# Kernel optimization log

Hardware: AMD Instinct MI355X
Metric: run time of the kernel (lower is better)

## Reference

```python
import jax, jax.numpy as jnp
import numpy as np

NEG_INF = -1.0e9
LEAKY_SLOPE = 0.2


def setup_inputs() -> dict:
    key = jax.random.key(0)
    k1, k2, k3, k4, k5 = jax.random.split(key, 5)
    B, N, F_in, H, D = 4, 2048, 128, 4, 32
    x = jax.random.normal(k1, (B, N, F_in), dtype=jnp.float32)
    # binary adjacency; force self-loops so every row has >=1 neighbour
    adj = jax.random.randint(k2, (N, N), 0, 2).astype(jnp.float32)
    adj = jnp.maximum(adj, jnp.eye(N, dtype=jnp.float32))
    W = jax.random.normal(k3, (H, F_in, D), dtype=jnp.float32) * (1.0 / np.sqrt(F_in))
    a_left = jax.random.normal(k4, (H, D, 1), dtype=jnp.float32) * (1.0 / np.sqrt(D))
    a_right = jax.random.normal(k5, (H, D, 1), dtype=jnp.float32) * (1.0 / np.sqrt(D))
    bias = jnp.zeros((H, D), dtype=jnp.float32)
    return {"x": x, "adj": adj, "W": W, "a_left": a_left, "a_right": a_right, "bias": bias}


def reference(x, adj, W, a_left, a_right, bias):
    # x: (B,N,F) ; W: (H,F,D) -> h: (B,H,N,D)
    h = jnp.einsum('bnf,hfd->bhnd', x, W)
    # separable additive scores: (B,H,N)
    al = jnp.einsum('bhnd,hd->bhn', h, a_left[..., 0])
    ar = jnp.einsum('bhnd,hd->bhn', h, a_right[..., 0])
    e = al[:, :, :, None] + ar[:, :, None, :]          # (B,H,N,N)
    e = jnp.where(e >= 0, e, LEAKY_SLOPE * e)           # LeakyReLU(0.2)
    mask = adj[None, None] > 0.5
    e = jnp.where(mask, e, NEG_INF)
    alpha = jax.nn.softmax(e, axis=-1)                  # (B,H,N,N)
    # inference: dropout on alpha is identity
    out = jnp.einsum('bhmn,bhnd->bhmd', alpha, h) + bias[None, :, None, :]
    out = jax.nn.elu(out)
    # concat heads: (B,H,N,D) -> (B,N,H*D)
    B, H, N, D = out.shape
    out = jnp.transpose(out, (0, 2, 1, 3)).reshape(B, N, H * D)
    return out
```

## Files before the change

### kernel.cpp

```cpp
#include <hip/hip_runtime.h>
#include <hip/hip_bf16.h>

#define Bn 4
#define Nn 2048
#define Fn 128
#define Hn 4
#define Dn 32
#define LOG2E 1.44269504f

typedef __attribute__((ext_vector_type(4))) float f32x4;
typedef __attribute__((ext_vector_type(8))) short s16x8;
typedef __attribute__((ext_vector_type(4))) short s16x4;
typedef _Float16 f16x8 __attribute__((ext_vector_type(8)));

__device__ __forceinline__ short f2h(float f) {
  _Float16 h = (_Float16)f;
  return __builtin_bit_cast(short, h);
}

__global__ __launch_bounds__(256) void k_pack(
    const float* __restrict__ adj, const float* __restrict__ W,
    const float* __restrict__ aL, const float* __restrict__ aR,
    unsigned long long* __restrict__ adjbits, short* __restrict__ Wt,
    short* __restrict__ Waux)
{
  const int blk = blockIdx.x;
  const int t = threadIdx.x;
  if (blk < Nn) {
    const int wv = t >> 6, lane = t & 63;
    const float* ap = adj + (size_t)blk * Nn;
    #pragma unroll
    for (int s = 0; s < 8; ++s) {
      const int n0 = (wv * 8 + s) * 64;
      const unsigned long long m = __ballot(ap[n0 + lane] > 0.5f);
      if (lane == 0) adjbits[blk * 32 + wv * 8 + s] = m;
    }
  } else if (t < 128) {
    const int h = blk - Nn;
    const int f = t;
    const float* Wp = W + ((size_t)h * Fn + f) * Dn;
    float wv[32];
    float dl = 0.f, dr = 0.f;
    #pragma unroll
    for (int d4 = 0; d4 < 8; ++d4) {
      const f32x4 w4 = *(const f32x4*)(Wp + d4 * 4);
      #pragma unroll
      for (int j = 0; j < 4; ++j) {
        const int d = d4 * 4 + j;
        wv[d] = w4[j];
        dl = fmaf(w4[j], aL[h * Dn + d], dl);
        dr = fmaf(w4[j], aR[h * Dn + d], dr);
      }
    }
    #pragma unroll
    for (int d = 0; d < 32; ++d)
      Wt[(h * Dn + d) * Fn + f] = f2h(wv[d]);
    Waux[(h * 2 + 0) * Fn + f] = f2h(dl * LOG2E);
    Waux[(h * 2 + 1) * Fn + f] = f2h(dr * LOG2E);
    if (h == 0) {
      #pragma unroll
      for (int cc = 8; cc < 16; ++cc) Waux[cc * Fn + f] = 0;
    }
  }
}

__global__ void k_proj(
    const float* __restrict__ x, const short* __restrict__ Wt,
    const short* __restrict__ Waux,
    float* __restrict__ al, float* __restrict__ ar, short* __restrict__ ht)
{
  const int m0 = blockIdx.x * 16;
  const int b = m0 >> 11, nloc = m0 & 2047;
  const int lane = threadIdx.x;
  const int r = lane & 15, g = lane >> 4;

  const float* xp = x + (size_t)(m0 + r) * Fn + g * 8;
  f32x4 c[8] = {};
  f32x4 caux = {};
  #pragma unroll
  for (int ks = 0; ks < 4; ++ks) {
    const f32x4 xa = *(const f32x4*)(xp + ks * 32);
    const f32x4 xb = *(const f32x4*)(xp + ks * 32 + 4);
    f16x8 af;
    #pragma unroll
    for (int j = 0; j < 4; ++j) { af[j] = (_Float16)xa[j]; af[j + 4] = (_Float16)xb[j]; }
    const short* wp = Wt + r * Fn + ks * 32 + g * 8;
    #pragma unroll
    for (int cf = 0; cf < 8; ++cf) {
      const f16x8 bf = __builtin_bit_cast(f16x8, *(const s16x8*)(wp + cf * 16 * Fn));
      c[cf] = __builtin_amdgcn_mfma_f32_16x16x32_f16(af, bf, c[cf], 0, 0, 0);
    }
    const f16x8 ba = __builtin_bit_cast(f16x8, *(const s16x8*)(Waux + r * Fn + ks * 32 + g * 8));
    caux = __builtin_amdgcn_mfma_f32_16x16x32_f16(af, ba, caux, 0, 0, 0);
  }

  #pragma unroll
  for (int cf = 0; cf < 8; ++cf) {
    const int hd = cf >> 1, d = (cf & 1) * 16 + r;
    s16x4 hv;
    #pragma unroll
    for (int q = 0; q < 4; ++q) hv[q] = f2h(c[cf][q]);
    *(s16x4*)(ht + ((size_t)(b * Hn + hd) * Dn + d) * Nn + nloc + g * 4) = hv;
  }

  if (r < 8) {
    const int hh = r >> 1;
    float* dst = (r & 1) ? ar : al;
    #pragma unroll
    for (int q = 0; q < 4; ++q)
      dst[(size_t)(b * Hn + hh) * Nn + nloc + g * 4 + q] = caux[q];
  }
}

__global__ __launch_bounds__(512, 2) void k_attn(
    const unsigned long long* __restrict__ adjbits,
    const float* __restrict__ al, const float* __restrict__ ar,
    const short* __restrict__ ht, const float* __restrict__ bias,
    float* __restrict__ out)
{
  __shared__ float ar_s[32][68];
  __shared__ float accS[8][16][33];
  __shared__ float lS[8][16];

  const int blk = blockIdx.x;
  const int mt = blk & 127, bh = blk >> 7;
  const int b = bh >> 2, head = bh & 3;
  const int m0 = mt * 16;
  const int t = threadIdx.x;
  const int wv = t >> 6, lane = t & 63;
  const int r = lane & 15, g = lane >> 4;

  {
    const f32x4 av = ((const f32x4*)(ar + (size_t)bh * Nn))[t];
    *(f32x4*)&ar_s[t >> 4][(t & 15) * 4] = av;
  }

  const unsigned long long abits = adjbits[(size_t)(m0 + r) * 32 + wv * 4 + g];
  const float al_m = al[(size_t)bh * Nn + m0 + r] - 4.0f;

  const short* htA = ht + ((size_t)bh * Dn + r) * Nn + wv * 256 + g * 64;
  const short* htB = htA + 16 * Nn;
  s16x8 hA0 = *(const s16x8*)(htA);      s16x8 hB0 = *(const s16x8*)(htB);
  s16x8 hA1 = *(const s16x8*)(htA + 8);  s16x8 hB1 = *(const s16x8*)(htB + 8);
  s16x8 hA2 = *(const s16x8*)(htA + 16); s16x8 hB2 = *(const s16x8*)(htB + 16);
  s16x8 hA3 = *(const s16x8*)(htA + 24); s16x8 hB3 = *(const s16x8*)(htB + 24);
  s16x8 hA4 = *(const s16x8*)(htA + 32); s16x8 hB4 = *(const s16x8*)(htB + 32);
  s16x8 hA5 = *(const s16x8*)(htA + 40); s16x8 hB5 = *(const s16x8*)(htB + 40);
  s16x8 hA6 = *(const s16x8*)(htA + 48); s16x8 hB6 = *(const s16x8*)(htB + 48);
  s16x8 hA7 = *(const s16x8*)(htA + 56); s16x8 hB7 = *(const s16x8*)(htB + 56);
  asm volatile("" :: "v"(hA0), "v"(hA1), "v"(hA2), "v"(hA3),
                     "v"(hA4), "v"(hA5), "v"(hA6), "v"(hA7),
                     "v"(hB0), "v"(hB1), "v"(hB2), "v"(hB3),
                     "v"(hB4), "v"(hB5), "v"(hB6), "v"(hB7));

  __syncthreads();

  const float* arp = &ar_s[wv * 4 + g][0];
  f32x4 accA = {0.f,0.f,0.f,0.f}, accB = {0.f,0.f,0.f,0.f};
  f32x4 accL = {0.f,0.f,0.f,0.f};
  const f16x8 onesB = {(_Float16)1.f, (_Float16)1.f, (_Float16)1.f, (_Float16)1.f,
                       (_Float16)1.f, (_Float16)1.f, (_Float16)1.f, (_Float16)1.f};

  #define CHUNK(ci, hAx, hBx)                                                  \
  {                                                                            \
    const f32x4 a0 = *(const f32x4*)(arp + ci * 8);                            \
    const f32x4 a1 = *(const f32x4*)(arp + ci * 8 + 4);                        \
    const unsigned int byte = (unsigned int)(abits >> (ci * 8)) & 0xffu;       \
    float p[8];                                                                \
    _Pragma("unroll")                                                          \
    for (int j = 0; j < 4; ++j) {                                              \
      const float s0 = al_m + a0[j];                                           \
      const float s1 = al_m + a1[j];                                           \
      const float e0 = __builtin_amdgcn_exp2f(fmaxf(s0, fmaf(0.2f, s0, -3.2f))); \
      const float e1 = __builtin_amdgcn_exp2f(fmaxf(s1, fmaf(0.2f, s1, -3.2f))); \
      p[j]     = (byte & (1u << j))       ? e0 : 0.f;                          \
      p[j + 4] = (byte & (1u << (j + 4))) ? e1 : 0.f;                          \
    }                                                                          \
    f16x8 pf;                                                                  \
    _Pragma("unroll")                                                          \
    for (int j = 0; j < 8; ++j) pf[j] = (_Float16)p[j];                        \
    accA = __builtin_amdgcn_mfma_f32_16x16x32_f16(                             \
        pf, __builtin_bit_cast(f16x8, hAx), accA, 0, 0, 0);                    \
    accB = __builtin_amdgcn_mfma_f32_16x16x32_f16(                             \
        pf, __builtin_bit_cast(f16x8, hBx), accB, 0, 0, 0);                    \
    accL = __builtin_amdgcn_mfma_f32_16x16x32_f16(pf, onesB, accL, 0, 0, 0);   \
  }

  CHUNK(0, hA0, hB0) CHUNK(1, hA1, hB1) CHUNK(2, hA2, hB2) CHUNK(3, hA3, hB3)
  CHUNK(4, hA4, hB4) CHUNK(5, hA5, hB5) CHUNK(6, hA6, hB6) CHUNK(7, hA7, hB7)
  #undef CHUNK

  #pragma unroll
  for (int q = 0; q < 4; ++q) {
    accS[wv][4 * g + q][r]      = accA[q];
    accS[wv][4 * g + q][r + 16] = accB[q];
  }
  if (r == 0) {
    #pragma unroll
    for (int q = 0; q < 4; ++q) lS[wv][4 * g + q] = accL[q];
  }
  __syncthreads();

  const int row = t >> 5, dc = t & 31;
  float L = 0.f, v = 0.f;
  #pragma unroll
  for (int w = 0; w < 8; ++w) { L += lS[w][row]; v += accS[w][row][dc]; }
  v = v / L + bias[head * Dn + dc];
  v = v > 0.f ? v : __expf(v) - 1.f;
  out[((size_t)b * Nn + m0 + row) * (Hn * Dn) + head * Dn + dc] = v;
}

extern "C" void kernel_launch(void* const* d_in, const int* in_sizes, int n_in,
                              void* d_out, int out_size, void* d_ws, size_t ws_size,
                              hipStream_t stream) {
  const float* x    = (const float*)d_in[0];
  const float* adj  = (const float*)d_in[1];
  const float* W    = (const float*)d_in[2];
  const float* aL   = (const float*)d_in[3];
  const float* aR   = (const float*)d_in[4];
  const float* bias = (const float*)d_in[5];
  float* out = (float*)d_out;

  float* al = (float*)d_ws;
  float* ar = al + (Bn * Hn) * Nn;
  short* ht = (short*)(ar + (Bn * Hn) * Nn);
  unsigned long long* adjbits =
      (unsigned long long*)(ht + (size_t)(Bn * Hn) * Dn * Nn);
  short* Wt = (short*)(adjbits + Nn * (Nn / 64));
  short* Waux = Wt + (Hn * Dn) * Fn;

  hipLaunchKernelGGL(k_pack, dim3(Nn + Hn), dim3(256), 0, stream,
                     adj, W, aL, aR, adjbits, Wt, Waux);
  hipLaunchKernelGGL(k_proj, dim3((Bn * Nn) / 16), dim3(64), 0, stream,
                     x, Wt, Waux, al, ar, ht);
  hipLaunchKernelGGL(k_attn, dim3((Bn * Hn) * (Nn / 16)), dim3(512), 0, stream,
                     adjbits, al, ar, ht, bias, out);
}
```

Baseline: 122.5 us.

## Factor LeakyReLU-softmax exponentials into per-node fp16 terms and pipeline attention loads

The change uses exp(leaky(a+b)) = max(exp(a)exp(b), exp(0.2a)exp(0.2b)). The projection kernel now precomputes the per-node exp2 factors for the left and right scores and stores them in fp16. The attention kernel then builds each probability with packed fp16 multiplies, a max and a bitmask, instead of one transcendental per pair. Right-side factors and h tiles are fetched with hand-scheduled, double-buffered inline-asm global loads instead of LDS staging plus upfront register preloads, and occupancy hints are raised. The risks are reduced fp16 precision and range in the factored exponentials, and fragile hand-written vmcnt scheduling.

```diff
diff --git a/kernel.cpp b/kernel.cpp
--- a/kernel.cpp
+++ b/kernel.cpp
@@ -9,13 +9,16 @@
 #define LOG2E 1.44269504f
 
 typedef __attribute__((ext_vector_type(4))) float f32x4;
+typedef __attribute__((ext_vector_type(4))) int   i32x4;
 typedef __attribute__((ext_vector_type(8))) short s16x8;
 typedef __attribute__((ext_vector_type(4))) short s16x4;
 typedef _Float16 f16x8 __attribute__((ext_vector_type(8)));
 
-__device__ __forceinline__ short f2h(float f) {
+typedef unsigned int uint;
+
+__device__ __forceinline__ unsigned short f2h(float f) {
   _Float16 h = (_Float16)f;
-  return __builtin_bit_cast(short, h);
+  return __builtin_bit_cast(unsigned short, h);
 }
 
 __global__ __launch_bounds__(256) void k_pack(
@@ -54,9 +57,9 @@
     }
     #pragma unroll
     for (int d = 0; d < 32; ++d)
-      Wt[(h * Dn + d) * Fn + f] = f2h(wv[d]);
-    Waux[(h * 2 + 0) * Fn + f] = f2h(dl * LOG2E);
-    Waux[(h * 2 + 1) * Fn + f] = f2h(dr * LOG2E);
+      Wt[(h * Dn + d) * Fn + f] = (short)f2h(wv[d]);
+    Waux[(h * 2 + 0) * Fn + f] = (short)f2h(dl * LOG2E);
+    Waux[(h * 2 + 1) * Fn + f] = (short)f2h(dr * LOG2E);
     if (h == 0) {
       #pragma unroll
       for (int cc = 8; cc < 16; ++cc) Waux[cc * Fn + f] = 0;
@@ -64,10 +67,11 @@
   }
 }
 
-__global__ void k_proj(
+__global__ __launch_bounds__(64, 4) void k_proj(
     const float* __restrict__ x, const short* __restrict__ Wt,
     const short* __restrict__ Waux,
-    float* __restrict__ al, float* __restrict__ ar, short* __restrict__ ht)
+    uint* __restrict__ eafa, short* __restrict__ erh, short* __restrict__ frh,
+    short* __restrict__ ht)
 {
   const int m0 = blockIdx.x * 16;
   const int b = m0 >> 11, nloc = m0 & 2047;
@@ -99,26 +103,35 @@
     const int hd = cf >> 1, d = (cf & 1) * 16 + r;
     s16x4 hv;
     #pragma unroll
-    for (int q = 0; q < 4; ++q) hv[q] = f2h(c[cf][q]);
+    for (int q = 0; q < 4; ++q) hv[q] = (short)f2h(c[cf][q]);
     *(s16x4*)(ht + ((size_t)(b * Hn + hd) * Dn + d) * Nn + nloc + g * 4) = hv;
   }
 
   if (r < 8) {
-    const int hh = r >> 1;
-    float* dst = (r & 1) ? ar : al;
-    #pragma unroll
-    for (int q = 0; q < 4; ++q)
-      dst[(size_t)(b * Hn + hh) * Nn + nloc + g * 4 + q] = caux[q];
-  }
-}
-
-__global__ __launch_bounds__(512, 2) void k_attn(
+    const int hh = r >> 1, side = r & 1;
+    #pragma unroll
+    for (int q = 0; q < 4; ++q) {
+      const float v = caux[q];
+      const float Ev = __builtin_amdgcn_exp2f(v - 2.0f);
+      const float Fv = __builtin_amdgcn_exp2f(fmaf(0.2f, v, -2.0f));
+      const size_t idx = (size_t)(b * Hn + hh) * Nn + nloc + g * 4 + q;
+      if (side == 0) {
+        eafa[idx] = (uint)f2h(Ev) | ((uint)f2h(Fv) << 16);
+      } else {
+        erh[idx] = (short)f2h(Ev);
+        frh[idx] = (short)f2h(Fv);
+      }
+    }
+  }
+}
+
+__global__ __launch_bounds__(512, 4) void k_attn(
     const unsigned long long* __restrict__ adjbits,
-    const float* __restrict__ al, const float* __restrict__ ar,
+    const uint* __restrict__ eafa,
+    const short* __restrict__ erh, const short* __restrict__ frh,
     const short* __restrict__ ht, const float* __restrict__ bias,
     float* __restrict__ out)
 {
-  __shared__ float ar_s[32][68];
   __shared__ float accS[8][16][33];
   __shared__ float lS[8][16];
 
@@ -129,66 +142,75 @@
   const int t = threadIdx.x;
   const int wv = t >> 6, lane = t & 63;
   const int r = lane & 15, g = lane >> 4;
-
-  {
-    const f32x4 av = ((const f32x4*)(ar + (size_t)bh * Nn))[t];
-    *(f32x4*)&ar_s[t >> 4][(t & 15) * 4] = av;
-  }
+  const int nb = wv * 256 + g * 64;
 
   const unsigned long long abits = adjbits[(size_t)(m0 + r) * 32 + wv * 4 + g];
-  const float al_m = al[(size_t)bh * Nn + m0 + r] - 4.0f;
-
-  const short* htA = ht + ((size_t)bh * Dn + r) * Nn + wv * 256 + g * 64;
-  const short* htB = htA + 16 * Nn;
-  s16x8 hA0 = *(const s16x8*)(htA);      s16x8 hB0 = *(const s16x8*)(htB);
-  s16x8 hA1 = *(const s16x8*)(htA + 8);  s16x8 hB1 = *(const s16x8*)(htB + 8);
-  s16x8 hA2 = *(const s16x8*)(htA + 16); s16x8 hB2 = *(const s16x8*)(htB + 16);
-  s16x8 hA3 = *(const s16x8*)(htA + 24); s16x8 hB3 = *(const s16x8*)(htB + 24);
-  s16x8 hA4 = *(const s16x8*)(htA + 32); s16x8 hB4 = *(const s16x8*)(htB + 32);
-  s16x8 hA5 = *(const s16x8*)(htA + 40); s16x8 hB5 = *(const s16x8*)(htB + 40);
-  s16x8 hA6 = *(const s16x8*)(htA + 48); s16x8 hB6 = *(const s16x8*)(htB + 48);
-  s16x8 hA7 = *(const s16x8*)(htA + 56); s16x8 hB7 = *(const s16x8*)(htB + 56);
-  asm volatile("" :: "v"(hA0), "v"(hA1), "v"(hA2), "v"(hA3),
-                     "v"(hA4), "v"(hA5), "v"(hA6), "v"(hA7),
-                     "v"(hB0), "v"(hB1), "v"(hB2), "v"(hB3),
-                     "v"(hB4), "v"(hB5), "v"(hB6), "v"(hB7));
-
-  __syncthreads();
-
-  const float* arp = &ar_s[wv * 4 + g][0];
-  f32x4 accA = {0.f,0.f,0.f,0.f}, accB = {0.f,0.f,0.f,0.f};
-  f32x4 accL = {0.f,0.f,0.f,0.f};
-  const f16x8 onesB = {(_Float16)1.f, (_Float16)1.f, (_Float16)1.f, (_Float16)1.f,
-                       (_Float16)1.f, (_Float16)1.f, (_Float16)1.f, (_Float16)1.f};
-
-  #define CHUNK(ci, hAx, hBx)                                                  \
-  {                                                                            \
-    const f32x4 a0 = *(const f32x4*)(arp + ci * 8);                            \
-    const f32x4 a1 = *(const f32x4*)(arp + ci * 8 + 4);                        \
-    const unsigned int byte = (unsigned int)(abits >> (ci * 8)) & 0xffu;       \
-    float p[8];                                                                \
-    _Pragma("unroll")                                                          \
-    for (int j = 0; j < 4; ++j) {                                              \
-      const float s0 = al_m + a0[j];                                           \
-      const float s1 = al_m + a1[j];                                           \
-      const float e0 = __builtin_amdgcn_exp2f(fmaxf(s0, fmaf(0.2f, s0, -3.2f))); \
-      const float e1 = __builtin_amdgcn_exp2f(fmaxf(s1, fmaf(0.2f, s1, -3.2f))); \
-      p[j]     = (byte & (1u << j))       ? e0 : 0.f;                          \
-      p[j + 4] = (byte & (1u << (j + 4))) ? e1 : 0.f;                          \
-    }                                                                          \
-    f16x8 pf;                                                                  \
-    _Pragma("unroll")                                                          \
-    for (int j = 0; j < 8; ++j) pf[j] = (_Float16)p[j];                        \
-    accA = __builtin_amdgcn_mfma_f32_16x16x32_f16(                             \
-        pf, __builtin_bit_cast(f16x8, hAx), accA, 0, 0, 0);                    \
-    accB = __builtin_amdgcn_mfma_f32_16x16x32_f16(                             \
-        pf, __builtin_bit_cast(f16x8, hBx), accB, 0, 0, 0);                    \
-    accL = __builtin_amdgcn_mfma_f32_16x16x32_f16(pf, onesB, accL, 0, 0, 0);   \
-  }
-
-  CHUNK(0, hA0, hB0) CHUNK(1, hA1, hB1) CHUNK(2, hA2, hB2) CHUNK(3, hA3, hB3)
-  CHUNK(4, hA4, hB4) CHUNK(5, hA5, hB5) CHUNK(6, hA6, hB6) CHUNK(7, hA7, hB7)
-  #undef CHUNK
+  const uint ef = eafa[(size_t)bh * Nn + m0 + r];
+  uint ea2 = ef & 0xFFFFu;  ea2 |= ea2 << 16;
+  uint fa2 = ef >> 16;      fa2 |= fa2 << 16;
+  const i32x4 ea4 = {(int)ea2, (int)ea2, (int)ea2, (int)ea2};
+  const i32x4 fa4 = {(int)fa2, (int)fa2, (int)fa2, (int)fa2};
+  const f16x8 EA8 = __builtin_bit_cast(f16x8, ea4);
+  const f16x8 FA8 = __builtin_bit_cast(f16x8, fa4);
+  const f16x8 ones = {(_Float16)1.f, (_Float16)1.f, (_Float16)1.f, (_Float16)1.f,
+                      (_Float16)1.f, (_Float16)1.f, (_Float16)1.f, (_Float16)1.f};
+
+  const unsigned long long er_p = (unsigned long long)(erh + (size_t)bh * Nn + nb);
+  const unsigned long long fr_p = (unsigned long long)(frh + (size_t)bh * Nn + nb);
+  const unsigned long long ha_p = (unsigned long long)(ht + ((size_t)bh * Dn + r) * Nn + nb);
+  const unsigned long long hb_p = ha_p + (size_t)(16 * Nn) * 2;
+
+  f32x4 accA = {0.f,0.f,0.f,0.f}, accB = {0.f,0.f,0.f,0.f}, accL = {0.f,0.f,0.f,0.f};
+
+  asm volatile("" :: "v"(ea4), "v"(fa4), "v"(abits));
+  asm volatile("s_waitcnt vmcnt(0)");
+  __builtin_amdgcn_sched_barrier(0);
+
+  i32x4 b0_er, b0_fr, b0_ha, b0_hb;
+  i32x4 b1_er, b1_fr, b1_ha, b1_hb;
+
+  #define GLD(dst, base, OFF) \
+    asm volatile("global_load_dwordx4 %0, %1, off offset:" OFF \
+                 : "=v"(dst) : "v"(base))
+  #define ISSUE(BUF, OFF) \
+    GLD(BUF##_er, er_p, OFF); GLD(BUF##_fr, fr_p, OFF); \
+    GLD(BUF##_ha, ha_p, OFF); GLD(BUF##_hb, hb_p, OFF);
+  #define VWAIT(N) \
+    asm volatile("s_waitcnt vmcnt(" #N ")"); __builtin_amdgcn_sched_barrier(0)
+
+  #define PM(bb, j) (((uint)(((int)((bb) << (31 - 2*(j)))) >> 31) & 0xFFFFu) | \
+                     ((uint)(((int)((bb) << (30 - 2*(j)))) >> 31) << 16))
+
+  #define COMPUTE(ci, BUF) { \
+    const f16x8 E = __builtin_bit_cast(f16x8, BUF##_er) * EA8; \
+    const f16x8 F = __builtin_bit_cast(f16x8, BUF##_fr) * FA8; \
+    f16x8 P = __builtin_elementwise_max(E, F); \
+    i32x4 pu = __builtin_bit_cast(i32x4, P); \
+    const uint bb = (uint)(abits >> (8 * ci)) & 0xffu; \
+    pu[0] &= (int)PM(bb, 0); pu[1] &= (int)PM(bb, 1); \
+    pu[2] &= (int)PM(bb, 2); pu[3] &= (int)PM(bb, 3); \
+    P = __builtin_bit_cast(f16x8, pu); \
+    accA = __builtin_amdgcn_mfma_f32_16x16x32_f16(P, __builtin_bit_cast(f16x8, BUF##_ha), accA, 0, 0, 0); \
+    accB = __builtin_amdgcn_mfma_f32_16x16x32_f16(P, __builtin_bit_cast(f16x8, BUF##_hb), accB, 0, 0, 0); \
+    accL = __builtin_amdgcn_mfma_f32_16x16x32_f16(P, ones, accL, 0, 0, 0); \
+  }
+
+  ISSUE(b0, "0");  ISSUE(b1, "16");
+  VWAIT(4); COMPUTE(0, b0); ISSUE(b0, "32");
+  VWAIT(4); COMPUTE(1, b1); ISSUE(b1, "48");
+  VWAIT(4); COMPUTE(2, b0); ISSUE(b0, "64");
+  VWAIT(4); COMPUTE(3, b1); ISSUE(b1, "80");
+  VWAIT(4); COMPUTE(4, b0); ISSUE(b0, "96");
+  VWAIT(4); COMPUTE(5, b1); ISSUE(b1, "112");
+  VWAIT(4); COMPUTE(6, b0);
+  VWAIT(0); COMPUTE(7, b1);
+  __builtin_amdgcn_sched_barrier(0);
+
+  #undef GLD
+  #undef ISSUE
+  #undef VWAIT
+  #undef PM
+  #undef COMPUTE
 
   #pragma unroll
   for (int q = 0; q < 4; ++q) {
@@ -221,18 +243,19 @@
   const float* bias = (const float*)d_in[5];
   float* out = (float*)d_out;
 
-  float* al = (float*)d_ws;
-  float* ar = al + (Bn * Hn) * Nn;
-  short* ht = (short*)(ar + (Bn * Hn) * Nn);
+  uint*  eafa = (uint*)d_ws;
+  short* erh  = (short*)(eafa + (Bn * Hn) * Nn);
+  short* frh  = erh + (Bn * Hn) * Nn;
+  short* ht   = frh + (Bn * Hn) * Nn;
   unsigned long long* adjbits =
       (unsigned long long*)(ht + (size_t)(Bn * Hn) * Dn * Nn);
-  short* Wt = (short*)(adjbits + Nn * (Nn / 64));
+  short* Wt   = (short*)(adjbits + Nn * (Nn / 64));
   short* Waux = Wt + (Hn * Dn) * Fn;
 
   hipLaunchKernelGGL(k_pack, dim3(Nn + Hn), dim3(256), 0, stream,
                      adj, W, aL, aR, adjbits, Wt, Waux);
   hipLaunchKernelGGL(k_proj, dim3((Bn * Nn) / 16), dim3(64), 0, stream,
-                     x, Wt, Waux, al, ar, ht);
+                     x, Wt, Waux, eafa, erh, frh, ht);
   hipLaunchKernelGGL(k_attn, dim3((Bn * Hn) * (Nn / 16)), dim3(512), 0, stream,
-                     adjbits, al, ar, ht, bias, out);
-}
+                     adjbits, eafa, erh, frh, ht, bias, out);
+}
```

Measured after the change: 177.7 us. 1.45x slower.
